# Performance work log

Measured on AMD Instinct MI355X. Metric: run time of the kernel, lower is better.

## Reference

```python
import jax, jax.numpy as jnp
import numpy as np

B, L, D = 128, 196, 1024  # batch, att_size, rnn_size


def setup_inputs() -> dict:
    key = jax.random.key(0)
    ks = jax.random.split(key, 11)
    s = 1.0 / np.sqrt(D)
    return {
        "x": jax.random.normal(ks[0], (B, D), jnp.float32),
        "att": jax.random.normal(ks[1], (B, L, D), jnp.float32),
        "h": jax.random.normal(ks[2], (B, D), jnp.float32),
        "W_a2a": jax.random.uniform(ks[3], (D, D), jnp.float32, -s, s),
        "b_a2a": jax.random.uniform(ks[4], (D,), jnp.float32, -s, s),
        "W_h2a": jax.random.uniform(ks[5], (D, D), jnp.float32, -s, s),
        "b_h2a": jax.random.uniform(ks[6], (D,), jnp.float32, -s, s),
        "W_i2a": jax.random.uniform(ks[7], (D, D), jnp.float32, -s, s),
        "b_i2a": jax.random.uniform(ks[8], (D,), jnp.float32, -s, s),
        "W_d2d": jax.random.uniform(ks[9], (D,), jnp.float32, -s, s),
        "b_d2d": jax.random.uniform(ks[10], (), jnp.float32, -s, s),
    }


def reference(x, att, h, W_a2a, b_a2a, W_h2a, b_h2a, W_i2a, b_i2a, W_d2d, b_d2d):
    # att_v_1: [B, L, D]
    att_v = jnp.einsum('bld,ed->ble', att, W_a2a) + b_a2a
    att_h = (h @ W_h2a.T + b_h2a)[:, None, :]   # [B, 1, D]
    att_x = (x @ W_i2a.T + b_i2a)[:, None, :]   # [B, 1, D]
    dot = jnp.tanh(att_v + att_h + att_x)       # [B, L, D]
    scores = jnp.einsum('bld,d->bl', dot, W_d2d) + b_d2d  # [B, L]
    weight = jax.nn.softmax(scores, axis=-1)    # [B, L]
    att_res = jnp.einsum('bld,bl->bd', att, weight)  # [B, D]
    return att_res
```

## Files before the change

kernel.cpp:

```cpp
#include <hip/hip_runtime.h>
#include <hip/hip_bf16.h>

#define B_ 128
#define L_ 196
#define D_ 1024

typedef __attribute__((ext_vector_type(8))) short short8v;
typedef __attribute__((ext_vector_type(4))) float f32x4;
typedef unsigned short ushort_t;

#define OFF_ATTBF   0UL
#define OFF_WBF     51380224UL
#define OFF_A2      53477376UL
#define OFF_W2      54001664UL
#define OFF_SPART   53477376UL
#define OFF_CPART   58195968UL

__device__ inline unsigned short f2bf(float f) {
  unsigned int u = __float_as_uint(f);
  unsigned int r = (u + 0x7fffu + ((u >> 16) & 1u)) >> 16;
  return (unsigned short)r;
}

__global__ void convert_kernel(const float* __restrict__ att, const float* __restrict__ Wa,
                               const float* __restrict__ x,   const float* __restrict__ h,
                               const float* __restrict__ Wi,  const float* __restrict__ Wh,
                               ushort_t* __restrict__ att_bf, ushort_t* __restrict__ W_bf,
                               ushort_t* __restrict__ A2,     ushort_t* __restrict__ W2) {
  const int n0 = (B_*L_*D_)/4;
  const int n1 = (D_*D_)/4;
  const int n2 = (B_*D_)/4;
  const int total = n0 + n1 + 2*n2 + 2*n1;
  for (int idx = blockIdx.x*blockDim.x + threadIdx.x; idx < total;
       idx += gridDim.x*blockDim.x) {
    const float4* src; ushort_t* dst;
    int i = idx;
    if (i < n0)               { src = (const float4*)att + i; dst = att_bf + (size_t)i*4; }
    else if ((i -= n0) < n1)  { src = (const float4*)Wa  + i; dst = W_bf  + (size_t)i*4; }
    else if ((i -= n1) < n2)  { int b = i>>8, k4 = i&255; src = (const float4*)x  + i; dst = A2 + b*2048 + k4*4; }
    else if ((i -= n2) < n2)  { int b = i>>8, k4 = i&255; src = (const float4*)h  + i; dst = A2 + b*2048 + 1024 + k4*4; }
    else if ((i -= n2) < n1)  { int e = i>>8, k4 = i&255; src = (const float4*)Wi + i; dst = W2 + e*2048 + k4*4; }
    else { i -= n1;             int e = i>>8, k4 = i&255; src = (const float4*)Wh + i; dst = W2 + e*2048 + 1024 + k4*4; }
    float4 v = *src;
    ushort4 o; o.x = f2bf(v.x); o.y = f2bf(v.y); o.z = f2bf(v.z); o.w = f2bf(v.w);
    *(ushort4*)dst = o;
  }
}

__device__ inline void stage_tile(const ushort_t* __restrict__ g, int row0, int Kld, int k0,
                                  ushort_t* ldst, int t) {
  #pragma unroll
  for (int it = 0; it < 4; ++it) {
    int linear = it*4096 + t*16;
    int r = linear >> 7;
    int c = (t & 7) ^ (r & 7);
    const ushort_t* src = g + (size_t)(row0 + r)*Kld + k0 + c*8;
    ushort_t* dst = ldst + ((it*4096 + ((t & 192) << 4)) >> 1);
    __builtin_amdgcn_global_load_lds((const __attribute__((address_space(1))) void*)src,
                                     (__attribute__((address_space(3))) void*)dst,
                                     16, 0, 0);
  }
}

__device__ inline short8v ldfrag(const ushort_t* tile, int row, int c) {
  int phys = c ^ (row & 7);
  return *(const short8v*)(tile + row*64 + phys*8);
}

__global__ __launch_bounds__(256) void gemm_c_kernel(
    const ushort_t* __restrict__ Amat, const ushort_t* __restrict__ Bmat,
    float* __restrict__ cpart) {
  __shared__ ushort_t lds[32768];
  int bid = blockIdx.x;
  int e0 = (bid & 7)*128;
  int kc = bid >> 3;
  int kbeg = kc*512;
  const int Kld = 2048;
  int t = threadIdx.x, lane = t & 63, w = t >> 6;
  int wm = w >> 1, we = w & 1;
  int lrow = lane & 15;
  int lk = lane >> 4;

  f32x4 acc[4][4];
  #pragma unroll
  for (int i = 0; i < 4; ++i)
    #pragma unroll
    for (int j = 0; j < 4; ++j) acc[i][j] = (f32x4){0.f, 0.f, 0.f, 0.f};

  stage_tile(Amat, 0,  Kld, kbeg, lds, t);
  stage_tile(Bmat, e0, Kld, kbeg, lds + 8192, t);
  __syncthreads();

  const int nk = 8;
  for (int kt = 0; kt < nk; ++kt) {
    int cur = kt & 1;
    if (kt + 1 < nk) {
      stage_tile(Amat, 0,  Kld, kbeg + ((kt+1) << 6), lds + (cur^1)*16384, t);
      stage_tile(Bmat, e0, Kld, kbeg + ((kt+1) << 6), lds + (cur^1)*16384 + 8192, t);
    }
    const ushort_t* At = lds + cur*16384;
    const ushort_t* Bt = At + 8192;
    #pragma unroll
    for (int hh = 0; hh < 2; ++hh) {
      short8v af[4], bfv[4];
      #pragma unroll
      for (int i = 0; i < 4; ++i) af[i]  = ldfrag(At, wm*64 + i*16 + lrow, hh*4 + lk);
      #pragma unroll
      for (int j = 0; j < 4; ++j) bfv[j] = ldfrag(Bt, we*64 + j*16 + lrow, hh*4 + lk);
      #pragma unroll
      for (int i = 0; i < 4; ++i)
        #pragma unroll
        for (int j = 0; j < 4; ++j)
          acc[i][j] = __builtin_amdgcn_mfma_f32_16x16x32_bf16(af[i], bfv[j], acc[i][j], 0, 0, 0);
    }
    __syncthreads();
  }

  float* outc = cpart + (size_t)kc*131072;
  #pragma unroll
  for (int i = 0; i < 4; ++i) {
    int m = wm*64 + i*16 + lk*4;
    #pragma unroll
    for (int j = 0; j < 4; ++j) {
      int e = e0 + we*64 + j*16 + lrow;
      #pragma unroll
      for (int r = 0; r < 4; ++r)
        outc[(m + r)*1024 + e] = acc[i][j][r];
    }
  }
}

#define BARR()  __builtin_amdgcn_s_barrier()
#define VM0()   asm volatile("s_waitcnt vmcnt(0)" ::: "memory")

__device__ inline void stageS(const ushort_t* __restrict__ g, int k0, ushort_t* ldsbase, int t) {
  #pragma unroll
  for (int it = 0; it < 4; ++it) {
    int linear = it*4096 + t*16;
    int r = linear >> 7;
    int c = ((linear >> 4) & 7) ^ (r & 7);
    const ushort_t* src = g + (size_t)r*1024 + k0 + c*8;
    ushort_t* dst = ldsbase + ((it*4096 + ((t & 192) << 4)) >> 1);
    __builtin_amdgcn_global_load_lds((const __attribute__((address_space(1))) void*)src,
                                     (__attribute__((address_space(3))) void*)dst,
                                     16, 0, 0);
  }
}

__global__ __launch_bounds__(256) void gemm_score_kernel(
    const ushort_t* __restrict__ Amat, const ushort_t* __restrict__ Bmat,
    const float* __restrict__ cpart,
    const float* __restrict__ ba, const float* __restrict__ bh, const float* __restrict__ bi,
    const float* __restrict__ wd,
    float* __restrict__ spart) {
  __shared__ ushort_t lds[16384];
  __shared__ float c_lds[256];
  int bid = blockIdx.x;
  int swz = (bid & 7)*196 + (bid >> 3);
  int m_blk = swz >> 3, n_blk = swz & 7;
  int m0 = m_blk*128, e0 = n_blk*128;
  int t = (int)threadIdx.x, lane = t & 63, w = t >> 6;
  int wm = w >> 1, we = w & 1;
  int lrow = lane & 15, lk = lane >> 4;

  int bb0 = m0 / 196;
  {
    int bb = bb0 + (t >> 7);
    int e  = e0 + (t & 127);
    float v = ba[e] + bh[e] + bi[e];
    if (bb < 128) {
      v += cpart[bb*1024 + e] + cpart[131072 + bb*1024 + e]
         + cpart[262144 + bb*1024 + e] + cpart[393216 + bb*1024 + e];
    }
    c_lds[t] = v;
  }

  const ushort_t* aG = Amat + (size_t)m0*1024;
  const ushort_t* bG = Bmat + (size_t)e0*1024;

  int lrow7 = lrow & 7;
  const ushort_t* pA0 = lds + (wm*64 + lrow)*64 + ((lk)     ^ lrow7)*8;
  const ushort_t* pA1 = lds + (wm*64 + lrow)*64 + (((4+lk)) ^ lrow7)*8;
  const ushort_t* pB0 = lds + 8192 + (we*64 + lrow)*64 + ((lk)     ^ lrow7)*8;
  const ushort_t* pB1 = lds + 8192 + (we*64 + lrow)*64 + (((4+lk)) ^ lrow7)*8;

  f32x4 acc[4][4];
  #pragma unroll
  for (int i = 0; i < 4; ++i)
    #pragma unroll
    for (int j = 0; j < 4; ++j) acc[i][j] = (f32x4){0.f, 0.f, 0.f, 0.f};

  stageS(aG, 0, lds, t);
  stageS(bG, 0, lds + 8192, t);

  for (int kt = 0; kt < 16; ++kt) {
    VM0();
    BARR();
    __builtin_amdgcn_s_setprio(1);
    #pragma unroll
    for (int ks = 0; ks < 2; ++ks) {
      const ushort_t* pa = ks ? pA1 : pA0;
      const ushort_t* pb = ks ? pB1 : pB0;
      short8v af[4], bfv[4];
      #pragma unroll
      for (int i = 0; i < 4; ++i) af[i]  = *(const short8v*)(pa + i*1024);
      #pragma unroll
      for (int j = 0; j < 4; ++j) bfv[j] = *(const short8v*)(pb + j*1024);
      #pragma unroll
      for (int i = 0; i < 4; ++i)
        #pragma unroll
        for (int j = 0; j < 4; ++j)
          acc[i][j] = __builtin_amdgcn_mfma_f32_16x16x32_bf16(af[i], bfv[j], acc[i][j], 0, 0, 0);
    }
    __builtin_amdgcn_s_setprio(0);
    BARR();
    if (kt < 15) {
      stageS(aG, (kt+1)*64, lds, t);
      stageS(bG, (kt+1)*64, lds + 8192, t);
    }
  }

  int p = n_blk*2 + we;
  #pragma unroll
  for (int i = 0; i < 4; ++i) {
    int mbase = m0 + wm*64 + i*16 + lk*4;
    f32x4 ps;
    #pragma unroll
    for (int r = 0; r < 4; ++r) {
      int m = mbase + r;
      int bb = (int)((unsigned)m / 196u);
      float partial = 0.f;
      #pragma unroll
      for (int j = 0; j < 4; ++j) {
        int ee = we*64 + j*16 + lrow;
        float v = acc[i][j][r] + c_lds[(bb - bb0)*128 + ee];
        float ex = __expf(2.f*v);
        partial += (1.f - 2.f/(ex + 1.f)) * wd[e0 + ee];
      }
      partial += __shfl_xor(partial, 1);
      partial += __shfl_xor(partial, 2);
      partial += __shfl_xor(partial, 4);
      partial += __shfl_xor(partial, 8);
      ps[r] = partial;
    }
    if (lrow == 0) *(f32x4*)(spart + (size_t)p*25088 + mbase) = ps;
  }
}

__global__ __launch_bounds__(256) void finalize_kernel(const ushort_t* __restrict__ att_bf,
                                                       const float* __restrict__ spart,
                                                       float* __restrict__ out) {
  int b  = blockIdx.x >> 1;
  int dh = blockIdx.x & 1;
  int t  = threadIdx.x;
  __shared__ float wls[L_];
  __shared__ float red[8];

  float s = -1e30f;
  if (t < L_) {
    int m = b*L_ + t;
    float sum = 0.f;
    #pragma unroll
    for (int p = 0; p < 16; ++p) sum += spart[p*25088 + m];
    s = sum;
  }
  float mx = s;
  #pragma unroll
  for (int off = 1; off < 64; off <<= 1) mx = fmaxf(mx, __shfl_xor(mx, off));
  if ((t & 63) == 0) red[t >> 6] = mx;
  __syncthreads();
  mx = fmaxf(fmaxf(red[0], red[1]), fmaxf(red[2], red[3]));
  float pr = (t < L_) ? __expf(s - mx) : 0.f;
  float ssum = pr;
  #pragma unroll
  for (int off = 1; off < 64; off <<= 1) ssum += __shfl_xor(ssum, off);
  if ((t & 63) == 0) red[4 + (t >> 6)] = ssum;
  __syncthreads();
  float tot = red[4] + red[5] + red[6] + red[7];
  if (t < L_) wls[t] = pr / tot;
  __syncthreads();

  int d = dh*512 + t*2;
  const ushort_t* abase = att_bf + (size_t)b*L_*D_ + d;
  float a0 = 0.f, a1 = 0.f;
  #pragma unroll 4
  for (int l = 0; l < L_; ++l) {
    float wv = wls[l];
    unsigned int v = *(const unsigned int*)(abase + (size_t)l*D_);
    float lo = __uint_as_float(v << 16);
    float hi = __uint_as_float(v & 0xffff0000u);
    a0 += wv*lo; a1 += wv*hi;
  }
  float2 o; o.x = a0; o.y = a1;
  *(float2*)(out + (size_t)b*D_ + d) = o;
}

extern "C" void kernel_launch(void* const* d_in, const int* in_sizes, int n_in,
                              void* d_out, int out_size, void* d_ws, size_t ws_size,
                              hipStream_t stream) {
  (void)in_sizes; (void)n_in; (void)out_size; (void)ws_size;
  const float* x   = (const float*)d_in[0];
  const float* att = (const float*)d_in[1];
  const float* h   = (const float*)d_in[2];
  const float* Wa  = (const float*)d_in[3];
  const float* ba  = (const float*)d_in[4];
  const float* Wh  = (const float*)d_in[5];
  const float* bh  = (const float*)d_in[6];
  const float* Wi  = (const float*)d_in[7];
  const float* bi  = (const float*)d_in[8];
  const float* wd  = (const float*)d_in[9];

  char* ws = (char*)d_ws;
  ushort_t* att_bf = (ushort_t*)(ws + OFF_ATTBF);
  ushort_t* W_bf   = (ushort_t*)(ws + OFF_WBF);
  ushort_t* A2     = (ushort_t*)(ws + OFF_A2);
  ushort_t* W2     = (ushort_t*)(ws + OFF_W2);
  float*    cpart  = (float*)(ws + OFF_CPART);
  float*    spart  = (float*)(ws + OFF_SPART);
  float*    out    = (float*)d_out;

  hipLaunchKernelGGL(convert_kernel, dim3(2048), dim3(256), 0, stream,
                     att, Wa, x, h, Wi, Wh, att_bf, W_bf, A2, W2);
  hipLaunchKernelGGL(gemm_c_kernel, dim3(32), dim3(256), 0, stream,
                     A2, W2, cpart);
  hipLaunchKernelGGL(gemm_score_kernel, dim3(1568), dim3(256), 0, stream,
                     att_bf, W_bf, cpart, ba, bh, bi, wd, spart);
  hipLaunchKernelGGL(finalize_kernel, dim3(256), dim3(256), 0, stream,
                     att_bf, spart, out);
}
```

Baseline: 127.7 us.

## Fuse fp32-to-bf16 conversion into small GEMM, widen convert and finalize loads

The small x/h projection GEMM now reads fp32 inputs directly and converts to bf16 while staging into LDS, so convert_kernel no longer writes and re-reads concatenated A2/W2 buffers. The GEMM is split over 64 blocks with 8 K-partials, and the score kernel sums all eight. convert_kernel handles 8 elements per thread with 16-byte stores. finalize splits L across four wave groups, each doing 16-byte loads, then reduces the partials through LDS. The small GEMM loses its async double-buffered global_load_lds pipeline in exchange.

```diff
diff --git a/kernel.cpp b/kernel.cpp
--- a/kernel.cpp
+++ b/kernel.cpp
@@ -11,10 +11,8 @@
 
 #define OFF_ATTBF   0UL
 #define OFF_WBF     51380224UL
-#define OFF_A2      53477376UL
-#define OFF_W2      54001664UL
 #define OFF_SPART   53477376UL
-#define OFF_CPART   58195968UL
+#define OFF_CPART   55083008UL
 
 __device__ inline unsigned short f2bf(float f) {
   unsigned int u = __float_as_uint(f);
@@ -23,42 +21,22 @@
 }
 
 __global__ void convert_kernel(const float* __restrict__ att, const float* __restrict__ Wa,
-                               const float* __restrict__ x,   const float* __restrict__ h,
-                               const float* __restrict__ Wi,  const float* __restrict__ Wh,
-                               ushort_t* __restrict__ att_bf, ushort_t* __restrict__ W_bf,
-                               ushort_t* __restrict__ A2,     ushort_t* __restrict__ W2) {
-  const int n0 = (B_*L_*D_)/4;
-  const int n1 = (D_*D_)/4;
-  const int n2 = (B_*D_)/4;
-  const int total = n0 + n1 + 2*n2 + 2*n1;
+                               ushort_t* __restrict__ att_bf, ushort_t* __restrict__ W_bf) {
+  const int n0 = (B_*L_*D_)/8;
+  const int n1 = (D_*D_)/8;
+  const int total = n0 + n1;
   for (int idx = blockIdx.x*blockDim.x + threadIdx.x; idx < total;
        idx += gridDim.x*blockDim.x) {
-    const float4* src; ushort_t* dst;
-    int i = idx;
-    if (i < n0)               { src = (const float4*)att + i; dst = att_bf + (size_t)i*4; }
-    else if ((i -= n0) < n1)  { src = (const float4*)Wa  + i; dst = W_bf  + (size_t)i*4; }
-    else if ((i -= n1) < n2)  { int b = i>>8, k4 = i&255; src = (const float4*)x  + i; dst = A2 + b*2048 + k4*4; }
-    else if ((i -= n2) < n2)  { int b = i>>8, k4 = i&255; src = (const float4*)h  + i; dst = A2 + b*2048 + 1024 + k4*4; }
-    else if ((i -= n2) < n1)  { int e = i>>8, k4 = i&255; src = (const float4*)Wi + i; dst = W2 + e*2048 + k4*4; }
-    else { i -= n1;             int e = i>>8, k4 = i&255; src = (const float4*)Wh + i; dst = W2 + e*2048 + 1024 + k4*4; }
-    float4 v = *src;
-    ushort4 o; o.x = f2bf(v.x); o.y = f2bf(v.y); o.z = f2bf(v.z); o.w = f2bf(v.w);
-    *(ushort4*)dst = o;
-  }
-}
-
-__device__ inline void stage_tile(const ushort_t* __restrict__ g, int row0, int Kld, int k0,
-                                  ushort_t* ldst, int t) {
-  #pragma unroll
-  for (int it = 0; it < 4; ++it) {
-    int linear = it*4096 + t*16;
-    int r = linear >> 7;
-    int c = (t & 7) ^ (r & 7);
-    const ushort_t* src = g + (size_t)(row0 + r)*Kld + k0 + c*8;
-    ushort_t* dst = ldst + ((it*4096 + ((t & 192) << 4)) >> 1);
-    __builtin_amdgcn_global_load_lds((const __attribute__((address_space(1))) void*)src,
-                                     (__attribute__((address_space(3))) void*)dst,
-                                     16, 0, 0);
+    const float4* s; ushort_t* d;
+    if (idx < n0) { s = (const float4*)att + (size_t)idx*2; d = att_bf + (size_t)idx*8; }
+    else { int i = idx - n0; s = (const float4*)Wa + (size_t)i*2; d = W_bf + (size_t)i*8; }
+    float4 f0 = s[0], f1 = s[1];
+    short8v o;
+    o[0] = (short)f2bf(f0.x); o[1] = (short)f2bf(f0.y);
+    o[2] = (short)f2bf(f0.z); o[3] = (short)f2bf(f0.w);
+    o[4] = (short)f2bf(f1.x); o[5] = (short)f2bf(f1.y);
+    o[6] = (short)f2bf(f1.z); o[7] = (short)f2bf(f1.w);
+    *(short8v*)d = o;
   }
 }
 
@@ -68,18 +46,19 @@
 }
 
 __global__ __launch_bounds__(256) void gemm_c_kernel(
-    const ushort_t* __restrict__ Amat, const ushort_t* __restrict__ Bmat,
+    const float* __restrict__ x, const float* __restrict__ h,
+    const float* __restrict__ Wi, const float* __restrict__ Wh,
     float* __restrict__ cpart) {
-  __shared__ ushort_t lds[32768];
+  __shared__ ushort_t lds[16384];
   int bid = blockIdx.x;
   int e0 = (bid & 7)*128;
   int kc = bid >> 3;
-  int kbeg = kc*512;
-  const int Kld = 2048;
+  const float* Asrc = (kc < 4) ? x : h;
+  const float* Bsrc = (kc < 4) ? Wi : Wh;
+  int kb = (kc & 3)*256;
   int t = threadIdx.x, lane = t & 63, w = t >> 6;
   int wm = w >> 1, we = w & 1;
-  int lrow = lane & 15;
-  int lk = lane >> 4;
+  int lrow = lane & 15, lk = lane >> 4;
 
   f32x4 acc[4][4];
   #pragma unroll
@@ -87,26 +66,34 @@
     #pragma unroll
     for (int j = 0; j < 4; ++j) acc[i][j] = (f32x4){0.f, 0.f, 0.f, 0.f};
 
-  stage_tile(Amat, 0,  Kld, kbeg, lds, t);
-  stage_tile(Bmat, e0, Kld, kbeg, lds + 8192, t);
-  __syncthreads();
-
-  const int nk = 8;
-  for (int kt = 0; kt < nk; ++kt) {
-    int cur = kt & 1;
-    if (kt + 1 < nk) {
-      stage_tile(Amat, 0,  Kld, kbeg + ((kt+1) << 6), lds + (cur^1)*16384, t);
-      stage_tile(Bmat, e0, Kld, kbeg + ((kt+1) << 6), lds + (cur^1)*16384 + 8192, t);
-    }
-    const ushort_t* At = lds + cur*16384;
-    const ushort_t* Bt = At + 8192;
+  for (int kt = 0; kt < 4; ++kt) {
+    int k0 = kb + (kt << 6);
+    #pragma unroll
+    for (int q = 0; q < 4; ++q) {
+      int li = t*4 + q;
+      int r = li >> 3, c = li & 7;
+      int phys = (c ^ (r & 7))*8;
+      const float* sA = Asrc + r*1024 + k0 + c*8;
+      float4 a0 = *(const float4*)sA, a1 = *(const float4*)(sA + 4);
+      short8v oa;
+      oa[0]=(short)f2bf(a0.x); oa[1]=(short)f2bf(a0.y); oa[2]=(short)f2bf(a0.z); oa[3]=(short)f2bf(a0.w);
+      oa[4]=(short)f2bf(a1.x); oa[5]=(short)f2bf(a1.y); oa[6]=(short)f2bf(a1.z); oa[7]=(short)f2bf(a1.w);
+      *(short8v*)(lds + r*64 + phys) = oa;
+      const float* sB = Bsrc + (size_t)(e0 + r)*1024 + k0 + c*8;
+      float4 b0 = *(const float4*)sB, b1 = *(const float4*)(sB + 4);
+      short8v ob;
+      ob[0]=(short)f2bf(b0.x); ob[1]=(short)f2bf(b0.y); ob[2]=(short)f2bf(b0.z); ob[3]=(short)f2bf(b0.w);
+      ob[4]=(short)f2bf(b1.x); ob[5]=(short)f2bf(b1.y); ob[6]=(short)f2bf(b1.z); ob[7]=(short)f2bf(b1.w);
+      *(short8v*)(lds + 8192 + r*64 + phys) = ob;
+    }
+    __syncthreads();
     #pragma unroll
     for (int hh = 0; hh < 2; ++hh) {
       short8v af[4], bfv[4];
       #pragma unroll
-      for (int i = 0; i < 4; ++i) af[i]  = ldfrag(At, wm*64 + i*16 + lrow, hh*4 + lk);
-      #pragma unroll
-      for (int j = 0; j < 4; ++j) bfv[j] = ldfrag(Bt, we*64 + j*16 + lrow, hh*4 + lk);
+      for (int i = 0; i < 4; ++i) af[i]  = ldfrag(lds, wm*64 + i*16 + lrow, hh*4 + lk);
+      #pragma unroll
+      for (int j = 0; j < 4; ++j) bfv[j] = ldfrag(lds + 8192, we*64 + j*16 + lrow, hh*4 + lk);
       #pragma unroll
       for (int i = 0; i < 4; ++i)
         #pragma unroll
@@ -169,8 +156,8 @@
     int e  = e0 + (t & 127);
     float v = ba[e] + bh[e] + bi[e];
     if (bb < 128) {
-      v += cpart[bb*1024 + e] + cpart[131072 + bb*1024 + e]
-         + cpart[262144 + bb*1024 + e] + cpart[393216 + bb*1024 + e];
+      #pragma unroll
+      for (int p = 0; p < 8; ++p) v += cpart[p*131072 + bb*1024 + e];
     }
     c_lds[t] = v;
   }
@@ -255,6 +242,7 @@
   int t  = threadIdx.x;
   __shared__ float wls[L_];
   __shared__ float red[8];
+  __shared__ float pacc[4][8][64];
 
   float s = -1e30f;
   if (t < L_) {
@@ -280,19 +268,33 @@
   if (t < L_) wls[t] = pr / tot;
   __syncthreads();
 
-  int d = dh*512 + t*2;
-  const ushort_t* abase = att_bf + (size_t)b*L_*D_ + d;
-  float a0 = 0.f, a1 = 0.f;
-  #pragma unroll 4
-  for (int l = 0; l < L_; ++l) {
-    float wv = wls[l];
-    unsigned int v = *(const unsigned int*)(abase + (size_t)l*D_);
-    float lo = __uint_as_float(v << 16);
-    float hi = __uint_as_float(v & 0xffff0000u);
-    a0 += wv*lo; a1 += wv*hi;
-  }
-  float2 o; o.x = a0; o.y = a1;
-  *(float2*)(out + (size_t)b*D_ + d) = o;
+  int dsub = t & 63, lg = t >> 6;
+  const ushort_t* abase = att_bf + (size_t)b*L_*D_ + dh*512 + dsub*8
+                        + (size_t)lg*49*D_;
+  float a0=0.f,a1=0.f,a2=0.f,a3=0.f,a4=0.f,a5=0.f,a6=0.f,a7=0.f;
+  #pragma unroll 7
+  for (int li = 0; li < 49; ++li) {
+    float wv = wls[lg*49 + li];
+    uint4 v = *(const uint4*)(abase + (size_t)li*D_);
+    a0 += wv*__uint_as_float(v.x << 16); a1 += wv*__uint_as_float(v.x & 0xffff0000u);
+    a2 += wv*__uint_as_float(v.y << 16); a3 += wv*__uint_as_float(v.y & 0xffff0000u);
+    a4 += wv*__uint_as_float(v.z << 16); a5 += wv*__uint_as_float(v.z & 0xffff0000u);
+    a6 += wv*__uint_as_float(v.w << 16); a7 += wv*__uint_as_float(v.w & 0xffff0000u);
+  }
+  pacc[lg][0][dsub] = a0; pacc[lg][1][dsub] = a1;
+  pacc[lg][2][dsub] = a2; pacc[lg][3][dsub] = a3;
+  pacc[lg][4][dsub] = a4; pacc[lg][5][dsub] = a5;
+  pacc[lg][6][dsub] = a6; pacc[lg][7][dsub] = a7;
+  __syncthreads();
+  if (t < 64) {
+    float o[8];
+    #pragma unroll
+    for (int j = 0; j < 8; ++j)
+      o[j] = pacc[0][j][t] + pacc[1][j][t] + pacc[2][j][t] + pacc[3][j][t];
+    float* ob = out + (size_t)b*D_ + dh*512 + t*8;
+    *(f32x4*)ob       = (f32x4){o[0], o[1], o[2], o[3]};
+    *(f32x4*)(ob + 4) = (f32x4){o[4], o[5], o[6], o[7]};
+  }
 }
 
 extern "C" void kernel_launch(void* const* d_in, const int* in_sizes, int n_in,
@@ -313,16 +315,14 @@
   char* ws = (char*)d_ws;
   ushort_t* att_bf = (ushort_t*)(ws + OFF_ATTBF);
   ushort_t* W_bf   = (ushort_t*)(ws + OFF_WBF);
-  ushort_t* A2     = (ushort_t*)(ws + OFF_A2);
-  ushort_t* W2     = (ushort_t*)(ws + OFF_W2);
+  float*    spart  = (float*)(ws + OFF_SPART);
   float*    cpart  = (float*)(ws + OFF_CPART);
-  float*    spart  = (float*)(ws + OFF_SPART);
   float*    out    = (float*)d_out;
 
   hipLaunchKernelGGL(convert_kernel, dim3(2048), dim3(256), 0, stream,
-                     att, Wa, x, h, Wi, Wh, att_bf, W_bf, A2, W2);
-  hipLaunchKernelGGL(gemm_c_kernel, dim3(32), dim3(256), 0, stream,
-                     A2, W2, cpart);
+                     att, Wa, att_bf, W_bf);
+  hipLaunchKernelGGL(gemm_c_kernel, dim3(64), dim3(256), 0, stream,
+                     x, h, Wi, Wh, cpart);
   hipLaunchKernelGGL(gemm_score_kernel, dim3(1568), dim3(256), 0, stream,
                      att_bf, W_bf, cpart, ba, bh, bi, wd, spart);
   hipLaunchKernelGGL(finalize_kernel, dim3(256), dim3(256), 0, stream,
```

Measured after the change: 127.4 us. Within noise of the previous version (-0.2%).
